# Kernel optimization log

Hardware: AMD Instinct MI355X
Metric: run time of the kernel (lower is better)

The kernel has to match this reference:

```python
import jax, jax.numpy as jnp
import numpy as np

N_NODES = 100000
D_SRC = 128
D_DST = 128
D_OUT = 256
N_EDGES = 600000


def setup_inputs() -> dict:
    key = jax.random.key(0)
    k1, k2, k3, k4, k5 = jax.random.split(key, 5)
    x_src = jax.random.normal(k1, (N_NODES, D_SRC), dtype=jnp.float32)
    x_dst = jax.random.normal(k2, (N_NODES, D_DST), dtype=jnp.float32)
    edge_index = jax.random.randint(k3, (2, N_EDGES), 0, N_NODES, dtype=jnp.int64)
    # Linear(in_src + in_dst, out): torch stores W as [out, in]
    fan_in = D_SRC + D_DST
    bound = 1.0 / np.sqrt(fan_in)
    W = jax.random.uniform(k4, (D_OUT, fan_in), minval=-bound, maxval=bound, dtype=jnp.float32)
    b = jax.random.uniform(k5, (D_OUT,), minval=-bound, maxval=bound, dtype=jnp.float32)
    return {"x_src": x_src, "x_dst": x_dst, "edge_index": edge_index, "W": W, "b": b}


def reference(x_src, x_dst, edge_index, W, b):
    src_idx, dst_idx = edge_index[0], edge_index[1]
    n_dst = x_dst.shape[0]
    x_j = x_src[src_idx]                                  # [E, D_SRC] gather
    summed = jax.ops.segment_sum(x_j, dst_idx, num_segments=n_dst)   # [N, D_SRC]
    count = jax.ops.segment_sum(jnp.ones((src_idx.shape[0],), dtype=x_src.dtype),
                                dst_idx, num_segments=n_dst)          # [N]
    agg = summed / jnp.maximum(count, 1.0)[:, None]        # scatter-mean
    h = jnp.concatenate([x_dst, agg], axis=-1)             # [N, D_DST+D_SRC]
    return jax.nn.relu(h @ W.T + b)                        # [N, D_OUT]
```

## Files before the change

### kernel.cpp

```cpp
#include <hip/hip_runtime.h>

#define N_NODES 100000
#define D_SRC 128
#define D_OUT 256
#define K_DIM 256
#define CAP 32
#define OVF_CAP 2048

typedef __attribute__((ext_vector_type(8))) short short8;
typedef __attribute__((ext_vector_type(4))) float float4v;

__device__ inline unsigned short f2bf(float f) {
    unsigned int u = __float_as_uint(f);
    u += 0x7FFF + ((u >> 16) & 1);
    return (unsigned short)(u >> 16);
}
__device__ inline float bf_lo(unsigned int u) { return __uint_as_float(u << 16); }
__device__ inline float bf_hi(unsigned int u) { return __uint_as_float(u & 0xFFFF0000u); }

__global__ __launch_bounds__(256) void bucket_kernel(
    const int* __restrict__ ei,
    int* __restrict__ deg,
    int* __restrict__ ovf_cnt,
    int* __restrict__ ovf,
    int* __restrict__ bucket,
    int n_edges)
{
    int e = blockIdx.x * 256 + threadIdx.x;
    if (e >= n_edges) return;
    int s = ei[e];
    int d = ei[n_edges + e];
    int pos = atomicAdd(deg + d, 1);
    if (pos < CAP) {
        bucket[(size_t)d * CAP + pos] = s;
    } else {
        int o = atomicAdd(ovf_cnt, 1);
        if (o < OVF_CAP) { ovf[2 * o] = s; ovf[2 * o + 1] = d; }
    }
}

__global__ __launch_bounds__(256) void pack_src_kernel(
    const float* __restrict__ x, unsigned short* __restrict__ xb)
{
    int i = blockIdx.x * 256 + threadIdx.x;
    float4 v = ((const float4*)x)[i];
    ushort4 o;
    o.x = f2bf(v.x); o.y = f2bf(v.y); o.z = f2bf(v.z); o.w = f2bf(v.w);
    ((ushort4*)xb)[i] = o;
}

__global__ __launch_bounds__(256) void convert_w_kernel(
    const float* __restrict__ W, unsigned short* __restrict__ Wb)
{
    int i = blockIdx.x * 256 + threadIdx.x;
    float4 v = ((const float4*)W)[i];
    ushort4 o;
    o.x = f2bf(v.x); o.y = f2bf(v.y); o.z = f2bf(v.z); o.w = f2bf(v.w);
    ((ushort4*)Wb)[i] = o;
}

__global__ __launch_bounds__(256) void gather_kernel(
    const unsigned short* __restrict__ xsb,
    const int*   __restrict__ deg,
    const int*   __restrict__ bucket,
    const int*   __restrict__ ovf_cnt,
    const int*   __restrict__ ovf,
    unsigned short* __restrict__ aggb)
{
    int node = blockIdx.x * 4 + (threadIdx.x >> 6);
    if (node >= N_NODES) return;
    int lane = threadIdx.x & 63;

    int dtot = deg[node];
    int n = (dtot < CAP) ? dtot : CAP;

    int idx = bucket[(size_t)node * CAP + (lane & 31)];

    float ax = 0.f, ay = 0.f;
    int i = 0;
    for (; i + 4 <= n; i += 4) {
        int s0 = __shfl(idx, i);
        int s1 = __shfl(idx, i + 1);
        int s2 = __shfl(idx, i + 2);
        int s3 = __shfl(idx, i + 3);
        unsigned int u0 = ((const unsigned int*)(xsb + (size_t)s0 * D_SRC))[lane];
        unsigned int u1 = ((const unsigned int*)(xsb + (size_t)s1 * D_SRC))[lane];
        unsigned int u2 = ((const unsigned int*)(xsb + (size_t)s2 * D_SRC))[lane];
        unsigned int u3 = ((const unsigned int*)(xsb + (size_t)s3 * D_SRC))[lane];
        ax += bf_lo(u0) + bf_lo(u1) + bf_lo(u2) + bf_lo(u3);
        ay += bf_hi(u0) + bf_hi(u1) + bf_hi(u2) + bf_hi(u3);
    }
    for (; i < n; ++i) {
        int s0 = __shfl(idx, i);
        unsigned int u0 = ((const unsigned int*)(xsb + (size_t)s0 * D_SRC))[lane];
        ax += bf_lo(u0);
        ay += bf_hi(u0);
    }

    if (dtot > CAP) {
        int oc = *ovf_cnt;
        if (oc > OVF_CAP) oc = OVF_CAP;
        for (int o = 0; o < oc; ++o) {
            if (ovf[2 * o + 1] == node) {
                int s0 = ovf[2 * o];
                unsigned int u0 = ((const unsigned int*)(xsb + (size_t)s0 * D_SRC))[lane];
                ax += bf_lo(u0);
                ay += bf_hi(u0);
            }
        }
    }

    float inv = 1.0f / (float)((dtot > 1) ? dtot : 1);
    unsigned int packed = (unsigned int)f2bf(ax * inv)
                        | ((unsigned int)f2bf(ay * inv) << 16);
    ((unsigned int*)(aggb + (size_t)node * D_SRC))[lane] = packed;
}

__global__ __launch_bounds__(256) void mfma_gemm_kernel(
    const float* __restrict__ x_dst,
    const unsigned short* __restrict__ aggb,
    const unsigned short* __restrict__ Wb,
    const float* __restrict__ bias,
    float*       __restrict__ out)
{
    __shared__ float eps[4][16][68];

    int wave = threadIdx.x >> 6;
    int lane = threadIdx.x & 63;
    int lrow = lane & 15;
    int kq   = lane >> 4;
    int m0 = blockIdx.x * 64;
    int n0 = wave * 64;

    float4v acc[4][4];
    #pragma unroll
    for (int i = 0; i < 4; ++i)
        #pragma unroll
        for (int j = 0; j < 4; ++j)
            acc[i][j] = (float4v){0.f, 0.f, 0.f, 0.f};

    int  rowv[4];
    bool rok[4];
    #pragma unroll
    for (int mf = 0; mf < 4; ++mf) {
        rowv[mf] = m0 + mf * 16 + lrow;
        rok[mf]  = rowv[mf] < N_NODES;
    }

    const short8 zfrag = (short8){0,0,0,0,0,0,0,0};

    #pragma unroll
    for (int kc = 0; kc < 8; ++kc) {
        const int k0 = kc * 32;
        short8 afrag[4], bfrag[4];

        if (kc < 4) {
            #pragma unroll
            for (int mf = 0; mf < 4; ++mf) {
                float4 v0 = make_float4(0.f, 0.f, 0.f, 0.f);
                float4 v1 = v0;
                if (rok[mf]) {
                    const float* p = x_dst + (size_t)rowv[mf] * D_SRC + k0 + kq * 8;
                    v0 = *(const float4*)p;
                    v1 = *(const float4*)(p + 4);
                }
                union { unsigned short s[8]; short8 v; } pk;
                pk.s[0] = f2bf(v0.x); pk.s[1] = f2bf(v0.y);
                pk.s[2] = f2bf(v0.z); pk.s[3] = f2bf(v0.w);
                pk.s[4] = f2bf(v1.x); pk.s[5] = f2bf(v1.y);
                pk.s[6] = f2bf(v1.z); pk.s[7] = f2bf(v1.w);
                afrag[mf] = pk.v;
            }
        } else {
            #pragma unroll
            for (int mf = 0; mf < 4; ++mf)
                afrag[mf] = rok[mf]
                    ? *(const short8*)(aggb + (size_t)rowv[mf] * D_SRC + (k0 - 128) + kq * 8)
                    : zfrag;
        }

        #pragma unroll
        for (int nf = 0; nf < 4; ++nf)
            bfrag[nf] = *(const short8*)(Wb + (size_t)(n0 + nf * 16 + lrow) * K_DIM + k0 + kq * 8);

        #pragma unroll
        for (int mf = 0; mf < 4; ++mf)
            #pragma unroll
            for (int nf = 0; nf < 4; ++nf)
                acc[mf][nf] = __builtin_amdgcn_mfma_f32_16x16x32_bf16(
                    afrag[mf], bfrag[nf], acc[mf][nf], 0, 0, 0);
    }

    float bv[4];
    #pragma unroll
    for (int nf = 0; nf < 4; ++nf)
        bv[nf] = bias[n0 + nf * 16 + lrow];

    int srow   = lane >> 4;
    int schunk = lane & 15;

    #pragma unroll
    for (int mf = 0; mf < 4; ++mf) {
        #pragma unroll
        for (int nf = 0; nf < 4; ++nf)
            #pragma unroll
            for (int r = 0; r < 4; ++r)
                eps[wave][kq * 4 + r][nf * 16 + lrow] =
                    fmaxf(acc[mf][nf][r] + bv[nf], 0.f);
        __syncthreads();
        #pragma unroll
        for (int c = 0; c < 4; ++c) {
            int row  = c * 4 + srow;
            float4 v = *(const float4*)&eps[wave][row][schunk * 4];
            int grow = m0 + mf * 16 + row;
            if (grow < N_NODES)
                *(float4*)(out + (size_t)grow * D_OUT + n0 + schunk * 4) = v;
        }
        __syncthreads();
    }
}

extern "C" void kernel_launch(void* const* d_in, const int* in_sizes, int n_in,
                              void* d_out, int out_size, void* d_ws, size_t ws_size,
                              hipStream_t stream) {
    const float* x_src = (const float*)d_in[0];
    const float* x_dst = (const float*)d_in[1];
    const int*   ei    = (const int*)d_in[2];
    const float* W     = (const float*)d_in[3];
    const float* bias  = (const float*)d_in[4];
    float* out = (float*)d_out;

    int n_edges = in_sizes[2] / 2;

    int* deg     = (int*)d_ws;
    int* ovf_cnt = deg + N_NODES;
    int* ovf     = ovf_cnt + 4;
    int* bucket  = ovf + OVF_CAP * 2;
    unsigned short* aggb = (unsigned short*)(bucket + (size_t)N_NODES * CAP);
    unsigned short* Wb   = aggb + (size_t)N_NODES * D_SRC;
    unsigned short* xsb  = Wb + (size_t)D_OUT * K_DIM;

    hipMemsetAsync(d_ws, 0, (N_NODES + 4) * sizeof(int), stream);

    bucket_kernel<<<(n_edges + 255) / 256, 256, 0, stream>>>(
        ei, deg, ovf_cnt, ovf, bucket, n_edges);

    pack_src_kernel<<<(N_NODES * D_SRC / 4) / 256, 256, 0, stream>>>(x_src, xsb);

    convert_w_kernel<<<(D_OUT * K_DIM / 4) / 256, 256, 0, stream>>>(W, Wb);

    gather_kernel<<<(N_NODES + 3) / 4, 256, 0, stream>>>(
        xsb, deg, bucket, ovf_cnt, ovf, aggb);

    mfma_gemm_kernel<<<(N_NODES + 63) / 64, 256, 0, stream>>>(
        x_dst, aggb, Wb, bias, out);
}
```

Before: 332.8 us.

## Fuse gather into GEMM via LDS and merge bucketing with bf16 packing

The mean-aggregation gather now runs inside the GEMM kernel. Each block gathers its 64 node rows into padded shared memory, which removes the aggregated-feature round trip through global memory. The edge bucketing and the bf16 conversions of x_src, x_dst and W are merged into one launch, cutting the kernel count from five to two. x_dst is now pre-converted to bf16 in a separate pass, which adds a write and read of that array. Gather latency is also now serialized before the MFMA phase within each block, with only one wave per 16 rows, so overlap depends on occupancy.

```diff
diff --git a/kernel.cpp b/kernel.cpp
--- a/kernel.cpp
+++ b/kernel.cpp
@@ -6,6 +6,7 @@
 #define K_DIM 256
 #define CAP 32
 #define OVF_CAP 2048
+#define PADA 136
 
 typedef __attribute__((ext_vector_type(8))) short short8;
 typedef __attribute__((ext_vector_type(4))) float float4v;
@@ -18,118 +19,114 @@
 __device__ inline float bf_lo(unsigned int u) { return __uint_as_float(u << 16); }
 __device__ inline float bf_hi(unsigned int u) { return __uint_as_float(u & 0xFFFF0000u); }
 
-__global__ __launch_bounds__(256) void bucket_kernel(
-    const int* __restrict__ ei,
+__global__ __launch_bounds__(256) void bucket_pack_kernel(
+    const int*   __restrict__ ei,
+    const float* __restrict__ x_src,
+    const float* __restrict__ x_dst,
+    const float* __restrict__ W,
     int* __restrict__ deg,
     int* __restrict__ ovf_cnt,
     int* __restrict__ ovf,
     int* __restrict__ bucket,
-    int n_edges)
+    unsigned short* __restrict__ xsb,
+    unsigned short* __restrict__ xdb,
+    unsigned short* __restrict__ Wb,
+    int n_edges, int eblocks)
 {
-    int e = blockIdx.x * 256 + threadIdx.x;
-    if (e >= n_edges) return;
-    int s = ei[e];
-    int d = ei[n_edges + e];
-    int pos = atomicAdd(deg + d, 1);
-    if (pos < CAP) {
-        bucket[(size_t)d * CAP + pos] = s;
+    if ((int)blockIdx.x < eblocks) {
+        int e = blockIdx.x * 256 + threadIdx.x;
+        if (e >= n_edges) return;
+        int s = ei[e];
+        int d = ei[n_edges + e];
+        int pos = atomicAdd(deg + d, 1);
+        if (pos < CAP) {
+            bucket[(size_t)d * CAP + pos] = s;
+        } else {
+            int o = atomicAdd(ovf_cnt, 1);
+            if (o < OVF_CAP) { ovf[2 * o] = s; ovf[2 * o + 1] = d; }
+        }
     } else {
-        int o = atomicAdd(ovf_cnt, 1);
-        if (o < OVF_CAP) { ovf[2 * o] = s; ovf[2 * o + 1] = d; }
-    }
-}
-
-__global__ __launch_bounds__(256) void pack_src_kernel(
-    const float* __restrict__ x, unsigned short* __restrict__ xb)
-{
-    int i = blockIdx.x * 256 + threadIdx.x;
-    float4 v = ((const float4*)x)[i];
-    ushort4 o;
-    o.x = f2bf(v.x); o.y = f2bf(v.y); o.z = f2bf(v.z); o.w = f2bf(v.w);
-    ((ushort4*)xb)[i] = o;
-}
-
-__global__ __launch_bounds__(256) void convert_w_kernel(
-    const float* __restrict__ W, unsigned short* __restrict__ Wb)
-{
-    int i = blockIdx.x * 256 + threadIdx.x;
-    float4 v = ((const float4*)W)[i];
-    ushort4 o;
-    o.x = f2bf(v.x); o.y = f2bf(v.y); o.z = f2bf(v.z); o.w = f2bf(v.w);
-    ((ushort4*)Wb)[i] = o;
-}
-
-__global__ __launch_bounds__(256) void gather_kernel(
+        const int NF = N_NODES * (D_SRC / 4);
+        const int WF = (D_OUT * K_DIM) / 4;
+        int i = (blockIdx.x - eblocks) * 256 + threadIdx.x;
+        const float* src; unsigned short* dst; int j;
+        if (i < NF)          { src = x_src; dst = xsb; j = i; }
+        else if (i < 2 * NF) { src = x_dst; dst = xdb; j = i - NF; }
+        else                 { j = i - 2 * NF; if (j >= WF) return; src = W; dst = Wb; }
+        float4 v = ((const float4*)src)[j];
+        ushort4 o;
+        o.x = f2bf(v.x); o.y = f2bf(v.y); o.z = f2bf(v.z); o.w = f2bf(v.w);
+        ((ushort4*)dst)[j] = o;
+    }
+}
+
+__global__ __launch_bounds__(256) void fused_gather_gemm_kernel(
     const unsigned short* __restrict__ xsb,
+    const unsigned short* __restrict__ xdb,
+    const unsigned short* __restrict__ Wb,
+    const float* __restrict__ bias,
     const int*   __restrict__ deg,
     const int*   __restrict__ bucket,
     const int*   __restrict__ ovf_cnt,
     const int*   __restrict__ ovf,
-    unsigned short* __restrict__ aggb)
+    float*       __restrict__ out)
 {
-    int node = blockIdx.x * 4 + (threadIdx.x >> 6);
-    if (node >= N_NODES) return;
-    int lane = threadIdx.x & 63;
-
-    int dtot = deg[node];
-    int n = (dtot < CAP) ? dtot : CAP;
-
-    int idx = bucket[(size_t)node * CAP + (lane & 31)];
-
-    float ax = 0.f, ay = 0.f;
-    int i = 0;
-    for (; i + 4 <= n; i += 4) {
-        int s0 = __shfl(idx, i);
-        int s1 = __shfl(idx, i + 1);
-        int s2 = __shfl(idx, i + 2);
-        int s3 = __shfl(idx, i + 3);
-        unsigned int u0 = ((const unsigned int*)(xsb + (size_t)s0 * D_SRC))[lane];
-        unsigned int u1 = ((const unsigned int*)(xsb + (size_t)s1 * D_SRC))[lane];
-        unsigned int u2 = ((const unsigned int*)(xsb + (size_t)s2 * D_SRC))[lane];
-        unsigned int u3 = ((const unsigned int*)(xsb + (size_t)s3 * D_SRC))[lane];
-        ax += bf_lo(u0) + bf_lo(u1) + bf_lo(u2) + bf_lo(u3);
-        ay += bf_hi(u0) + bf_hi(u1) + bf_hi(u2) + bf_hi(u3);
-    }
-    for (; i < n; ++i) {
-        int s0 = __shfl(idx, i);
-        unsigned int u0 = ((const unsigned int*)(xsb + (size_t)s0 * D_SRC))[lane];
-        ax += bf_lo(u0);
-        ay += bf_hi(u0);
-    }
-
-    if (dtot > CAP) {
-        int oc = *ovf_cnt;
-        if (oc > OVF_CAP) oc = OVF_CAP;
-        for (int o = 0; o < oc; ++o) {
-            if (ovf[2 * o + 1] == node) {
-                int s0 = ovf[2 * o];
+    __shared__ __align__(16) unsigned short AsU[64 * PADA];
+
+    int t = threadIdx.x;
+    int wave = t >> 6;
+    int lane = t & 63;
+    int m0 = blockIdx.x * 64;
+
+    for (int ni = 0; ni < 16; ++ni) {
+        int nrow = wave * 16 + ni;
+        int node = m0 + nrow;
+        unsigned int packed = 0;
+        if (node < N_NODES) {
+            int dtot = deg[node];
+            int n = (dtot < CAP) ? dtot : CAP;
+            int idx = bucket[(size_t)node * CAP + (lane & 31)];
+            float ax = 0.f, ay = 0.f;
+            int i = 0;
+            for (; i + 4 <= n; i += 4) {
+                int s0 = __shfl(idx, i);
+                int s1 = __shfl(idx, i + 1);
+                int s2 = __shfl(idx, i + 2);
+                int s3 = __shfl(idx, i + 3);
+                unsigned int u0 = ((const unsigned int*)(xsb + (size_t)s0 * D_SRC))[lane];
+                unsigned int u1 = ((const unsigned int*)(xsb + (size_t)s1 * D_SRC))[lane];
+                unsigned int u2 = ((const unsigned int*)(xsb + (size_t)s2 * D_SRC))[lane];
+                unsigned int u3 = ((const unsigned int*)(xsb + (size_t)s3 * D_SRC))[lane];
+                ax += bf_lo(u0) + bf_lo(u1) + bf_lo(u2) + bf_lo(u3);
+                ay += bf_hi(u0) + bf_hi(u1) + bf_hi(u2) + bf_hi(u3);
+            }
+            for (; i < n; ++i) {
+                int s0 = __shfl(idx, i);
                 unsigned int u0 = ((const unsigned int*)(xsb + (size_t)s0 * D_SRC))[lane];
                 ax += bf_lo(u0);
                 ay += bf_hi(u0);
             }
-        }
-    }
-
-    float inv = 1.0f / (float)((dtot > 1) ? dtot : 1);
-    unsigned int packed = (unsigned int)f2bf(ax * inv)
-                        | ((unsigned int)f2bf(ay * inv) << 16);
-    ((unsigned int*)(aggb + (size_t)node * D_SRC))[lane] = packed;
-}
-
-__global__ __launch_bounds__(256) void mfma_gemm_kernel(
-    const float* __restrict__ x_dst,
-    const unsigned short* __restrict__ aggb,
-    const unsigned short* __restrict__ Wb,
-    const float* __restrict__ bias,
-    float*       __restrict__ out)
-{
-    __shared__ float eps[4][16][68];
-
-    int wave = threadIdx.x >> 6;
-    int lane = threadIdx.x & 63;
+            if (dtot > CAP) {
+                int oc = *ovf_cnt;
+                if (oc > OVF_CAP) oc = OVF_CAP;
+                for (int o = 0; o < oc; ++o) {
+                    if (ovf[2 * o + 1] == node) {
+                        int s0 = ovf[2 * o];
+                        unsigned int u0 = ((const unsigned int*)(xsb + (size_t)s0 * D_SRC))[lane];
+                        ax += bf_lo(u0);
+                        ay += bf_hi(u0);
+                    }
+                }
+            }
+            float inv = 1.0f / (float)((dtot > 1) ? dtot : 1);
+            packed = (unsigned int)f2bf(ax * inv) | ((unsigned int)f2bf(ay * inv) << 16);
+        }
+        ((unsigned int*)(AsU + nrow * PADA))[lane] = packed;
+    }
+    __syncthreads();
+
     int lrow = lane & 15;
     int kq   = lane >> 4;
-    int m0 = blockIdx.x * 64;
     int n0 = wave * 64;
 
     float4v acc[4][4];
@@ -146,7 +143,6 @@
         rowv[mf] = m0 + mf * 16 + lrow;
         rok[mf]  = rowv[mf] < N_NODES;
     }
-
     const short8 zfrag = (short8){0,0,0,0,0,0,0,0};
 
     #pragma unroll
@@ -156,27 +152,14 @@
 
         if (kc < 4) {
             #pragma unroll
-            for (int mf = 0; mf < 4; ++mf) {
-                float4 v0 = make_float4(0.f, 0.f, 0.f, 0.f);
-                float4 v1 = v0;
-                if (rok[mf]) {
-                    const float* p = x_dst + (size_t)rowv[mf] * D_SRC + k0 + kq * 8;
-                    v0 = *(const float4*)p;
-                    v1 = *(const float4*)(p + 4);
-                }
-                union { unsigned short s[8]; short8 v; } pk;
-                pk.s[0] = f2bf(v0.x); pk.s[1] = f2bf(v0.y);
-                pk.s[2] = f2bf(v0.z); pk.s[3] = f2bf(v0.w);
-                pk.s[4] = f2bf(v1.x); pk.s[5] = f2bf(v1.y);
-                pk.s[6] = f2bf(v1.z); pk.s[7] = f2bf(v1.w);
-                afrag[mf] = pk.v;
-            }
-        } else {
-            #pragma unroll
             for (int mf = 0; mf < 4; ++mf)
                 afrag[mf] = rok[mf]
-                    ? *(const short8*)(aggb + (size_t)rowv[mf] * D_SRC + (k0 - 128) + kq * 8)
+                    ? *(const short8*)(xdb + (size_t)rowv[mf] * D_SRC + k0 + kq * 8)
                     : zfrag;
+        } else {
+            #pragma unroll
+            for (int mf = 0; mf < 4; ++mf)
+                afrag[mf] = *(const short8*)&AsU[(mf * 16 + lrow) * PADA + (k0 - 128) + kq * 8];
         }
 
         #pragma unroll
@@ -190,7 +173,9 @@
                 acc[mf][nf] = __builtin_amdgcn_mfma_f32_16x16x32_bf16(
                     afrag[mf], bfrag[nf], acc[mf][nf], 0, 0, 0);
     }
-
+    __syncthreads();
+
+    float* eps = (float*)AsU;
     float bv[4];
     #pragma unroll
     for (int nf = 0; nf < 4; ++nf)
@@ -205,13 +190,13 @@
         for (int nf = 0; nf < 4; ++nf)
             #pragma unroll
             for (int r = 0; r < 4; ++r)
-                eps[wave][kq * 4 + r][nf * 16 + lrow] =
+                eps[(wave * 16 + kq * 4 + r) * 68 + nf * 16 + lrow] =
                     fmaxf(acc[mf][nf][r] + bv[nf], 0.f);
         __syncthreads();
         #pragma unroll
         for (int c = 0; c < 4; ++c) {
             int row  = c * 4 + srow;
-            float4 v = *(const float4*)&eps[wave][row][schunk * 4];
+            float4 v = *(const float4*)&eps[(wave * 16 + row) * 68 + schunk * 4];
             int grow = m0 + mf * 16 + row;
             if (grow < N_NODES)
                 *(float4*)(out + (size_t)grow * D_OUT + n0 + schunk * 4) = v;
@@ -236,22 +221,18 @@
     int* ovf_cnt = deg + N_NODES;
     int* ovf     = ovf_cnt + 4;
     int* bucket  = ovf + OVF_CAP * 2;
-    unsigned short* aggb = (unsigned short*)(bucket + (size_t)N_NODES * CAP);
-    unsigned short* Wb   = aggb + (size_t)N_NODES * D_SRC;
-    unsigned short* xsb  = Wb + (size_t)D_OUT * K_DIM;
+    unsigned short* xsb = (unsigned short*)(bucket + (size_t)N_NODES * CAP);
+    unsigned short* xdb = xsb + (size_t)N_NODES * D_SRC;
+    unsigned short* Wb  = xdb + (size_t)N_NODES * D_SRC;
 
     hipMemsetAsync(d_ws, 0, (N_NODES + 4) * sizeof(int), stream);
 
-    bucket_kernel<<<(n_edges + 255) / 256, 256, 0, stream>>>(
-        ei, deg, ovf_cnt, ovf, bucket, n_edges);
-
-    pack_src_kernel<<<(N_NODES * D_SRC / 4) / 256, 256, 0, stream>>>(x_src, xsb);
-
-    convert_w_kernel<<<(D_OUT * K_DIM / 4) / 256, 256, 0, stream>>>(W, Wb);
-
-    gather_kernel<<<(N_NODES + 3) / 4, 256, 0, stream>>>(
-        xsb, deg, bucket, ovf_cnt, ovf, aggb);
-
-    mfma_gemm_kernel<<<(N_NODES + 63) / 64, 256, 0, stream>>>(
-        x_dst, aggb, Wb, bias, out);
-}
+    int eblocks = (n_edges + 255) / 256;
+    int pblocks = (2 * N_NODES * (D_SRC / 4) + (D_OUT * K_DIM) / 4 + 255) / 256;
+    bucket_pack_kernel<<<eblocks + pblocks, 256, 0, stream>>>(
+        ei, x_src, x_dst, W, deg, ovf_cnt, ovf, bucket, xsb, xdb, Wb,
+        n_edges, eblocks);
+
+    fused_gather_gemm_kernel<<<(N_NODES + 63) / 64, 256, 0, stream>>>(
+        xsb, xdb, Wb, bias, deg, bucket, ovf_cnt, ovf, out);
+}
```

After: 339.4 us. No clear change (+2.0%).
